# Kernel tuning notes

Hardware: AMD Instinct MI355X
Metric: run time of the kernel (lower is better)

## Reference

```python
import jax, jax.numpy as jnp
import numpy as np

# dims: batch B, n_token T, token_codim D, spatial HxW; channels C = T*D
B, T, D, H, W = 8, 64, 4, 128, 128
C = T * D  # 256
HM1, HM2 = 16, 16  # half of n_modes = (32, 32), per-block kept Fourier modes
EPS = 1e-5  # torch InstanceNorm2d default eps


def setup_inputs() -> dict:
    key = jax.random.key(0)
    ks = jax.random.split(key, 11)
    f = jnp.float32
    sk = 1.0 / (D * D)   # spectral weight init scale (K/Q/V blocks)
    se = 1.0 / (C * C)   # spectral weight init scale (end block)
    return {
        "x": jax.random.normal(ks[0], (B, C, H, W), f),
        "kqv_w1r": jax.random.normal(ks[1], (3, D, D, HM1, HM2), f) * sk,
        "kqv_w1i": jax.random.normal(ks[2], (3, D, D, HM1, HM2), f) * sk,
        "kqv_w2r": jax.random.normal(ks[3], (3, D, D, HM1, HM2), f) * sk,
        "kqv_w2i": jax.random.normal(ks[4], (3, D, D, HM1, HM2), f) * sk,
        "kqv_skip": jax.random.normal(ks[5], (3, D, D), f) * (1.0 / D),
        "end_w1r": jax.random.normal(ks[6], (C, C, HM1, HM2), f) * se,
        "end_w1i": jax.random.normal(ks[7], (C, C, HM1, HM2), f) * se,
        "end_w2r": jax.random.normal(ks[8], (C, C, HM1, HM2), f) * se,
        "end_w2i": jax.random.normal(ks[9], (C, C, HM1, HM2), f) * se,
        "end_skip": jax.random.normal(ks[10], (C, C), f) * (1.0 / C),
    }


def _spectral_conv(x, w1, w2):
    # x: [N, Cin, H, W]; w1/w2: complex [Cin, Cout, HM1, HM2]
    xf = jnp.fft.rfft2(x, norm="forward")  # [N, Cin, H, W//2+1]
    top = jnp.einsum("bixy,ioxy->boxy", xf[:, :, :HM1, :HM2], w1)
    bot = jnp.einsum("bixy,ioxy->boxy", xf[:, :, -HM1:, :HM2], w2)
    out_ft = jnp.zeros((x.shape[0], w1.shape[1], x.shape[2], x.shape[3] // 2 + 1), jnp.complex64)
    out_ft = out_ft.at[:, :, :HM1, :HM2].set(top).at[:, :, -HM1:, :HM2].set(bot)
    return jnp.fft.irfft2(out_ft, s=(x.shape[2], x.shape[3]), norm="forward")


def _fno_block(x, w1, w2, skip):
    # single FNO layer: spectral conv + pointwise linear ('linear' fno_skip), no activation (n_layers=1)
    return _spectral_conv(x, w1, w2) + jnp.einsum("oi,bihw->bohw", skip, x)


def reference(x, kqv_w1r, kqv_w1i, kqv_w2r, kqv_w2i, kqv_skip,
              end_w1r, end_w1i, end_w2r, end_w2i, end_skip):
    # b (t d) h w -> (b t) d h w
    xr = x.reshape(B * T, D, H, W)
    w1 = (kqv_w1r + 1j * kqv_w1i).astype(jnp.complex64)
    w2 = (kqv_w2r + 1j * kqv_w2i).astype(jnp.complex64)
    # stacked K, Q, V FNO blocks over leading axis of size 3
    kqv = jax.vmap(lambda a, b, s: _fno_block(xr, a, b, s))(w1, w2, kqv_skip)  # [3, B*T, D, H, W]
    k, q, v = (t.reshape(B, T, D * H * W) for t in kqv)
    # scaled dot-product attention over tokens (n_head = 1)
    attn = jax.nn.softmax(jnp.einsum("btd,bsd->bts", q, k) / (D * H * W), axis=-1)
    out = jnp.einsum("bts,bsd->btd", attn, v).reshape(B, C, H, W)
    # InstanceNorm2d(affine=False) + exact gelu
    mu = out.mean((-2, -1), keepdims=True)
    var = out.var((-2, -1), keepdims=True)  # biased variance, as in torch eval-mode instance norm
    out = (out - mu) * jax.lax.rsqrt(var + EPS)
    out = jax.nn.gelu(out, approximate=False)
    e1 = (end_w1r + 1j * end_w1i).astype(jnp.complex64)
    e2 = (end_w2r + 1j * end_w2i).astype(jnp.complex64)
    return _fno_block(out, e1, e2, end_skip)
```

## Files before the change

### kernel.cpp

```cpp
#include <hip/hip_runtime.h>
#include <hip/hip_bf16.h>


#define PI2 6.28318530717958647692f

__device__ __forceinline__ float b2f(unsigned short u){ return __uint_as_float(((unsigned)u)<<16); }
__device__ __forceinline__ float lo2f(unsigned u){ return __uint_as_float(u<<16); }
__device__ __forceinline__ float hi2f(unsigned u){ return __uint_as_float(u & 0xffff0000u); }
__device__ __forceinline__ unsigned short f2b(float f){
  unsigned x = __float_as_uint(f);
  x += 0x7fffu + ((x>>16)&1u);
  return (unsigned short)(x>>16);
}
__device__ __forceinline__ unsigned pack2(float a, float b){
  return (unsigned)f2b(a) | ((unsigned)f2b(b)<<16);
}

template<bool F32>
__global__ __launch_bounds__(256)
void k_fwd_dft(const void* __restrict__ srcv,
               float* __restrict__ outr, float* __restrict__ outi)
{
  __shared__ unsigned short xs[16384];
  __shared__ float Xwr[2048], Xwi[2048];
  __shared__ float twc[128], tws[128];
  const int tid = threadIdx.x;
  const long plane = blockIdx.x;
  if (F32){
    const float4* p4 = (const float4*)((const float*)srcv + plane*16384);
    uint2* x2 = (uint2*)xs;
    for (int i=tid;i<4096;i+=256){
      float4 v = p4[i];
      x2[i] = make_uint2(pack2(v.x,v.y), pack2(v.z,v.w));
    }
  } else {
    const uint4* p4 = (const uint4*)((const unsigned short*)srcv + plane*16384);
    uint4* x4 = (uint4*)xs;
    for (int i=tid;i<2048;i+=256) x4[i] = p4[i];
  }
  if (tid < 128){
    float s,c; sincosf((float)tid*(PI2/128.0f), &s, &c);
    twc[tid]=c; tws[tid]=s;
  }
  __syncthreads();
  const unsigned* xu = (const unsigned*)xs;
  for (int o=tid; o<2048; o+=256){
    int h = o >> 4, kx = o & 15;
    const unsigned* row = xu + h*64;
    float ar=0.f, ai=0.f;
    int m0 = 0, m1 = kx;
    const int step = (2*kx) & 127;
    for (int w2=0; w2<64; ++w2){
      unsigned u = row[w2];
      float a0 = lo2f(u), a1 = hi2f(u);
      ar = fmaf(a0, twc[m0], ar); ai = fmaf(-a0, tws[m0], ai);
      ar = fmaf(a1, twc[m1], ar); ai = fmaf(-a1, tws[m1], ai);
      m0 = (m0 + step) & 127; m1 = (m1 + step) & 127;
    }
    Xwr[o]=ar; Xwi[o]=ai;
  }
  __syncthreads();
  for (int o=tid; o<512; o+=256){
    int kyi = o >> 4, kx = o & 15;
    int ky = (kyi < 16) ? kyi : (kyi + 96);
    float ar=0.f, ai=0.f;
    int m = 0;
    const int step = ky & 127;
    for (int h=0; h<128; ++h){
      float A = Xwr[h*16+kx], B = Xwi[h*16+kx];
      float c = twc[m], s = tws[m];
      ar = fmaf(A, c, fmaf( B, s, ar));
      ai = fmaf(B, c, fmaf(-A, s, ai));
      m = (m + step) & 127;
    }
    outr[plane*512+o] = ar * (1.f/16384.f);
    outi[plane*512+o] = ai * (1.f/16384.f);
  }
}

__global__ __launch_bounds__(256)
void k_kqv_synth(const float* __restrict__ xfr, const float* __restrict__ xfi,
                 const float* __restrict__ w1r, const float* __restrict__ w1i,
                 const float* __restrict__ w2r, const float* __restrict__ w2i,
                 const float* __restrict__ skw,
                 const float* __restrict__ x,
                 unsigned short* __restrict__ qkv, int blk_off)
{
  __shared__ float xr_s[2048], xi_s[2048];
  __shared__ float ofr[512], ofi[512];
  __shared__ float Zr[2048], Zi[2048];
  __shared__ float twc[128], tws[128];
  const int tid = threadIdx.x;
  const int slot = blockIdx.x >> 9;
  const int blk  = blk_off + slot;
  const int bt   = blockIdx.x & 511;
  for (int j=tid; j<2048; j+=256){
    xr_s[j] = xfr[(long)bt*2048 + j];
    xi_s[j] = xfi[(long)bt*2048 + j];
  }
  if (tid < 128){
    float s,c; sincosf((float)tid*(PI2/128.0f), &s, &c);
    twc[tid]=c; tws[tid]=s;
  }
  __syncthreads();
  for (int o=0; o<4; ++o){
    for (int m=tid; m<512; m+=256){
      const int top = (m < 256);
      const float* wr = top ? w1r : w2r;
      const float* wi = top ? w1i : w2i;
      const int off = top ? m : (m-256);
      float ar=0.f, ai=0.f;
      #pragma unroll
      for (int i=0;i<4;++i){
        int widx = ((blk*4+i)*4+o)*256 + off;
        float wre = wr[widx], wim = wi[widx];
        float xr = xr_s[i*512+m], xi = xi_s[i*512+m];
        ar += xr*wre - xi*wim;
        ai += xr*wim + xi*wre;
      }
      ofr[m]=ar; ofi[m]=ai;
    }
    __syncthreads();
    for (int z=tid; z<2048; z+=256){
      int h = z >> 4, kx = z & 15;
      float ar=0.f, ai=0.f;
      int m = 0;
      const int step = h;
      #pragma unroll
      for (int kyi=0; kyi<16; ++kyi){
        float A=ofr[kyi*16+kx], B=ofi[kyi*16+kx];
        float c=twc[m], s=tws[m];
        ar = fmaf(A,c,fmaf(-B,s,ar));
        ai = fmaf(A,s,fmaf( B,c,ai));
        m = (m+step)&127;
      }
      m = (112*h)&127;
      #pragma unroll
      for (int kyi=16; kyi<32; ++kyi){
        float A=ofr[kyi*16+kx], B=ofi[kyi*16+kx];
        float c=twc[m], s=tws[m];
        ar = fmaf(A,c,fmaf(-B,s,ar));
        ai = fmaf(A,s,fmaf( B,c,ai));
        m = (m+step)&127;
      }
      float sc = (kx==0) ? 1.f : 2.f;
      Zr[z]=ar*sc; Zi[z]=ai*sc;
    }
    __syncthreads();
    float sk0=skw[(blk*4+o)*4+0];
    float sk1=skw[(blk*4+o)*4+1];
    float sk2=skw[(blk*4+o)*4+2];
    float sk3=skw[(blk*4+o)*4+3];
    const float* xb = x + (long)bt*65536;
    unsigned short* ob = qkv + ((long)(slot*512+bt)*4 + o)*16384;
    for (int pix=tid; pix<16384; pix+=256){
      int h = pix >> 7, w = pix & 127;
      const float* Zrh = Zr + h*16;
      const float* Zih = Zi + h*16;
      float acc = Zrh[0];
      float cw = twc[w], sw = tws[w];
      float cr = cw, si = sw;
      #pragma unroll
      for (int kx=1; kx<16; ++kx){
        acc = fmaf(Zrh[kx], cr, fmaf(-Zih[kx], si, acc));
        float cr2 = cr*cw - si*sw;
        si = fmaf(cr, sw, si*cw);
        cr = cr2;
      }
      acc = fmaf(sk0, xb[pix        ], acc);
      acc = fmaf(sk1, xb[16384 + pix], acc);
      acc = fmaf(sk2, xb[32768 + pix], acc);
      acc = fmaf(sk3, xb[49152 + pix], acc);
      ob[pix] = f2b(acc);
    }
    __syncthreads();
  }
}

__global__ __launch_bounds__(256)
void k_attn_qk(const unsigned short* __restrict__ qkv, float* __restrict__ Sp)
{
  __shared__ unsigned qs[8192], ks[8192];
  const int tid = threadIdx.x;
  const int b = blockIdx.x >> 8, ch = blockIdx.x & 255;
  {
    const unsigned* qg = (const unsigned*)qkv + (long)(512 + b*64)*32768 + ch*128;
    const unsigned* kg = (const unsigned*)qkv + (long)(b*64)*32768 + ch*128;
    for (int i=tid; i<8192; i+=256){
      int t = i >> 7, j = i & 127;
      int sw = j*64 + ((t + j) & 63);
      qs[sw] = qg[(long)t*32768 + j];
      ks[sw] = kg[(long)t*32768 + j];
    }
  }
  __syncthreads();
  const int t0 = (tid >> 4) << 2, s0 = (tid & 15) << 2;
  float acc[16];
  #pragma unroll
  for (int i=0;i<16;++i) acc[i]=0.f;
  for (int j=0; j<128; ++j){
    const unsigned* qrow = qs + j*64;
    const unsigned* krow = ks + j*64;
    float ql[4], qh[4], kl[4], kh[4];
    #pragma unroll
    for (int r=0;r<4;++r){ unsigned u=qrow[(t0+r+j)&63]; ql[r]=lo2f(u); qh[r]=hi2f(u); }
    #pragma unroll
    for (int c=0;c<4;++c){ unsigned u=krow[(s0+c+j)&63]; kl[c]=lo2f(u); kh[c]=hi2f(u); }
    #pragma unroll
    for (int r=0;r<4;++r)
      #pragma unroll
      for (int c=0;c<4;++c)
        acc[r*4+c] = fmaf(ql[r], kl[c], fmaf(qh[r], kh[c], acc[r*4+c]));
  }
  float* out = Sp + (long)(b*256+ch)*4096;
  #pragma unroll
  for (int r=0;r<4;++r)
    #pragma unroll
    for (int c=0;c<4;++c)
      out[(t0+r)*64 + s0+c] = acc[r*4+c];
}

__global__ __launch_bounds__(64)
void k_softmax(const float* __restrict__ Sp, float* __restrict__ attn)
{
  const int s = threadIdx.x;
  const int b = blockIdx.x >> 6, t = blockIdx.x & 63;
  const float* base = Sp + (long)b*1048576 + t*64 + s;
  float acc = 0.f;
  for (int ch=0; ch<256; ++ch) acc += base[(long)ch*4096];
  acc *= (1.f/65536.f);
  float mx = acc;
  #pragma unroll
  for (int off=32; off; off>>=1) mx = fmaxf(mx, __shfl_xor(mx, off));
  float e = __expf(acc - mx);
  float sm = e;
  #pragma unroll
  for (int off=32; off; off>>=1) sm += __shfl_xor(sm, off);
  attn[(long)blockIdx.x*64 + s] = e / sm;
}

__global__ __launch_bounds__(256)
void k_attn_v(const unsigned short* __restrict__ qkv, const float* __restrict__ attn,
              unsigned short* __restrict__ outg)
{
  __shared__ float At[4096];
  const int tid = threadIdx.x;
  const int pt = blockIdx.x & 15, d = (blockIdx.x>>4)&3, b = blockIdx.x>>6;
  for (int i=tid; i<4096; i+=256){
    int s = i >> 6, t = i & 63;
    At[i] = attn[(long)b*4096 + t*64 + s];
  }
  __syncthreads();
  const unsigned short* vb0 = qkv + ((long)(b*64)*4 + d)*16384;
  unsigned short* ob0 = outg + ((long)b*256 + d)*16384;
  for (int pass=0; pass<4; ++pass){
    int p = pt*1024 + pass*256 + tid;
    float acc[64];
    #pragma unroll
    for (int t=0;t<64;++t) acc[t]=0.f;
    for (int s=0; s<64; ++s){
      float vv = b2f(vb0[(long)s*65536 + p]);
      const float4* ar = (const float4*)(At + s*64);
      #pragma unroll
      for (int t4=0; t4<16; ++t4){
        float4 a = ar[t4];
        acc[t4*4+0] = fmaf(a.x, vv, acc[t4*4+0]);
        acc[t4*4+1] = fmaf(a.y, vv, acc[t4*4+1]);
        acc[t4*4+2] = fmaf(a.z, vv, acc[t4*4+2]);
        acc[t4*4+3] = fmaf(a.w, vv, acc[t4*4+3]);
      }
    }
    #pragma unroll
    for (int t=0;t<64;++t) ob0[(long)t*65536 + p] = f2b(acc[t]);
  }
}

__global__ __launch_bounds__(256)
void k_stats(const unsigned short* __restrict__ outg, float* __restrict__ stats)
{
  const int tid = threadIdx.x;
  const long plane = blockIdx.x;
  const unsigned* p = (const unsigned*)(outg + plane*16384);
  float s=0.f, q=0.f;
  for (int i=tid; i<8192; i+=256){
    unsigned u = p[i];
    float a = lo2f(u), b = hi2f(u);
    s += a + b; q = fmaf(a,a,fmaf(b,b,q));
  }
  __shared__ float red[8];
  #pragma unroll
  for (int off=32; off; off>>=1){ s += __shfl_xor(s, off); q += __shfl_xor(q, off); }
  if ((tid & 63) == 0){ red[tid>>6] = s; red[4 + (tid>>6)] = q; }
  __syncthreads();
  if (tid == 0){
    float S = red[0]+red[1]+red[2]+red[3];
    float Q = red[4]+red[5]+red[6]+red[7];
    float mu = S * (1.f/16384.f);
    float var = Q * (1.f/16384.f) - mu*mu;
    stats[plane*2]   = mu;
    stats[plane*2+1] = rsqrtf(var + 1e-5f);
  }
}

__global__ __launch_bounds__(256)
void k_norm_gelu(unsigned short* __restrict__ outg, const float* __restrict__ stats)
{
  unsigned* p = (unsigned*)outg;
  int gi = blockIdx.x*256 + threadIdx.x;
  #pragma unroll
  for (int it=0; it<8; ++it){
    int idx = gi + it*2097152;
    int plane = idx >> 13;
    float mu = stats[plane*2], rs = stats[plane*2+1];
    unsigned u = p[idx];
    float a = (lo2f(u)-mu)*rs, b = (hi2f(u)-mu)*rs;
    a = 0.5f*a*(1.f + erff(a*0.70710678118654752f));
    b = 0.5f*b*(1.f + erff(b*0.70710678118654752f));
    p[idx] = pack2(a, b);
  }
}

__global__ __launch_bounds__(256)
void k_end_mix(const float* __restrict__ gfr, const float* __restrict__ gfi,
               const float* __restrict__ w1r, const float* __restrict__ w1i,
               const float* __restrict__ w2r, const float* __restrict__ w2i,
               float* __restrict__ efr, float* __restrict__ efi)
{
  __shared__ float2 gbuf[2048];
  const int tid = threadIdx.x;
  const int kyi = blockIdx.x >> 4, ot = blockIdx.x & 15;
  const int ol = tid >> 4, kx = tid & 15;
  const int o = ot*16 + ol;
  const float* wr = (kyi < 16) ? w1r : w2r;
  const float* wi = (kyi < 16) ? w1i : w2i;
  const int moff = (kyi & 15)*16 + kx;
  const int mode = kyi*16 + kx;
  float accr[8], acci[8];
  #pragma unroll
  for (int bb=0; bb<8; ++bb){ accr[bb]=0.f; acci[bb]=0.f; }
  for (int ic=0; ic<16; ++ic){
    __syncthreads();
    for (int e=tid; e<2048; e+=256){
      int ii = e >> 7, r = e & 127, bb = r >> 4, k2 = r & 15;
      long gidx = ((long)(bb*256 + ic*16 + ii))*512 + kyi*16 + k2;
      gbuf[e] = make_float2(gfr[gidx], gfi[gidx]);
    }
    __syncthreads();
    #pragma unroll 4
    for (int ii=0; ii<16; ++ii){
      int i = ic*16 + ii;
      long widx = ((long)i*256 + o)*256 + moff;
      float wre = wr[widx], wim = wi[widx];
      #pragma unroll
      for (int bb=0; bb<8; ++bb){
        float2 g = gbuf[ii*128 + bb*16 + kx];
        accr[bb] = fmaf(g.x, wre, fmaf(-g.y, wim, accr[bb]));
        acci[bb] = fmaf(g.x, wim, fmaf( g.y, wre, acci[bb]));
      }
    }
  }
  #pragma unroll
  for (int bb=0; bb<8; ++bb){
    long eidx = ((long)(bb*256 + o))*512 + mode;
    efr[eidx] = accr[bb];
    efi[eidx] = acci[bb];
  }
}

__global__ __launch_bounds__(256)
void k_end_skip_add(const unsigned short* __restrict__ g, const float* __restrict__ skw,
                    float* __restrict__ outp)
{
  __shared__ unsigned short sk[16384];
  const int tid = threadIdx.x;
  const int pt = blockIdx.x & 31, ot = (blockIdx.x>>5)&3, b = blockIdx.x>>7;
  for (int e=tid; e<16384; e+=256){
    int ol = e >> 8, i = e & 255;
    int grp = ol >> 4, w = ol & 15;
    sk[i*64 + (((grp + i)&3)<<4) + w] = f2b(skw[(long)(ot*64+ol)*256 + i]);
  }
  __syncthreads();
  const int to = tid >> 6, tp = tid & 63;
  float acc[16][8];
  #pragma unroll
  for (int j=0;j<16;++j)
    #pragma unroll
    for (int px=0;px<8;++px) acc[j][px]=0.f;
  const uint4* g4 = (const uint4*)g + (long)b*524288 + pt*64 + tp;
  const uint4* skv4 = (const uint4*)sk;
  for (int i=0; i<256; ++i){
    uint4 gv = g4[(long)i*2048];
    float gx[8];
    gx[0]=lo2f(gv.x); gx[1]=hi2f(gv.x); gx[2]=lo2f(gv.y); gx[3]=hi2f(gv.y);
    gx[4]=lo2f(gv.z); gx[5]=hi2f(gv.z); gx[6]=lo2f(gv.w); gx[7]=hi2f(gv.w);
    const uint4* skp = skv4 + i*8 + (((to + i)&3)<<1);
    uint4 s0 = skp[0], s1 = skp[1];
    float sv[16];
    sv[0]=lo2f(s0.x); sv[1]=hi2f(s0.x); sv[2]=lo2f(s0.y); sv[3]=hi2f(s0.y);
    sv[4]=lo2f(s0.z); sv[5]=hi2f(s0.z); sv[6]=lo2f(s0.w); sv[7]=hi2f(s0.w);
    sv[8]=lo2f(s1.x); sv[9]=hi2f(s1.x); sv[10]=lo2f(s1.y); sv[11]=hi2f(s1.y);
    sv[12]=lo2f(s1.z); sv[13]=hi2f(s1.z); sv[14]=lo2f(s1.w); sv[15]=hi2f(s1.w);
    #pragma unroll
    for (int j=0;j<16;++j)
      #pragma unroll
      for (int px=0;px<8;++px)
        acc[j][px] = fmaf(sv[j], gx[px], acc[j][px]);
  }
  #pragma unroll
  for (int j=0;j<16;++j){
    int o = ot*64 + to*16 + j;
    long base = ((long)(b*256 + o))*16384 + pt*512 + tp*8;
    float4* ov = (float4*)(outp + base);
    ov[0] = make_float4(acc[j][0], acc[j][1], acc[j][2], acc[j][3]);
    ov[1] = make_float4(acc[j][4], acc[j][5], acc[j][6], acc[j][7]);
  }
}

__global__ __launch_bounds__(256)
void k_end_idft(const float* __restrict__ efr, const float* __restrict__ efi,
                float* __restrict__ outp)
{
  __shared__ float ofr[512], ofi[512];
  __shared__ float Zr[2048], Zi[2048];
  __shared__ float twc[128], tws[128];
  const int tid = threadIdx.x;
  const long plane = blockIdx.x;
  for (int m=tid; m<512; m+=256){ ofr[m]=efr[plane*512+m]; ofi[m]=efi[plane*512+m]; }
  if (tid < 128){
    float s,c; sincosf((float)tid*(PI2/128.0f), &s, &c);
    twc[tid]=c; tws[tid]=s;
  }
  __syncthreads();
  for (int z=tid; z<2048; z+=256){
    int h = z >> 4, kx = z & 15;
    float ar=0.f, ai=0.f;
    int m = 0;
    const int step = h;
    #pragma unroll
    for (int kyi=0; kyi<16; ++kyi){
      float A=ofr[kyi*16+kx], B=ofi[kyi*16+kx];
      float c=twc[m], s=tws[m];
      ar = fmaf(A,c,fmaf(-B,s,ar));
      ai = fmaf(A,s,fmaf( B,c,ai));
      m = (m+step)&127;
    }
    m = (112*h)&127;
    #pragma unroll
    for (int kyi=16; kyi<32; ++kyi){
      float A=ofr[kyi*16+kx], B=ofi[kyi*16+kx];
      float c=twc[m], s=tws[m];
      ar = fmaf(A,c,fmaf(-B,s,ar));
      ai = fmaf(A,s,fmaf( B,c,ai));
      m = (m+step)&127;
    }
    float sc = (kx==0) ? 1.f : 2.f;
    Zr[z]=ar*sc; Zi[z]=ai*sc;
  }
  __syncthreads();
  for (int pix=tid; pix<16384; pix+=256){
    int h = pix >> 7, w = pix & 127;
    const float* Zrh = Zr + h*16;
    const float* Zih = Zi + h*16;
    float acc = Zrh[0];
    float cw = twc[w], sw = tws[w];
    float cr = cw, si = sw;
    #pragma unroll
    for (int kx=1; kx<16; ++kx){
      acc = fmaf(Zrh[kx], cr, fmaf(-Zih[kx], si, acc));
      float cr2 = cr*cw - si*sw;
      si = fmaf(cr, sw, si*cw);
      cr = cr2;
    }
    outp[plane*16384 + pix] += acc;
  }
}

extern "C" void kernel_launch(void* const* d_in, const int* in_sizes, int n_in,
                              void* d_out, int out_size, void* d_ws, size_t ws_size,
                              hipStream_t stream) {
  const float* x     = (const float*)d_in[0];
  const float* kw1r  = (const float*)d_in[1];
  const float* kw1i  = (const float*)d_in[2];
  const float* kw2r  = (const float*)d_in[3];
  const float* kw2i  = (const float*)d_in[4];
  const float* kskip = (const float*)d_in[5];
  const float* ew1r  = (const float*)d_in[6];
  const float* ew1i  = (const float*)d_in[7];
  const float* ew2r  = (const float*)d_in[8];
  const float* ew2i  = (const float*)d_in[9];
  const float* eskip = (const float*)d_in[10];
  float* outp = (float*)d_out;

  unsigned short* qkv = (unsigned short*)d_out;

  char* ws = (char*)d_ws;
  float* XFr   = (float*)ws;
  float* XFi   = XFr + 1048576;
  float* Sp    = XFi + 1048576;
  float* EFr   = Sp;
  float* EFi   = Sp + 1048576;
  float* attn  = Sp + 8388608;
  float* stats = attn + 32768;
  unsigned short* outg = (unsigned short*)(stats + 4096);

  k_fwd_dft<true>  <<<2048, 256, 0, stream>>>(x, XFr, XFi);
  k_kqv_synth      <<<1024, 256, 0, stream>>>(XFr, XFi, kw1r, kw1i, kw2r, kw2i, kskip, x, qkv, 0);
  k_attn_qk        <<<2048, 256, 0, stream>>>(qkv, Sp);
  k_softmax        <<< 512,  64, 0, stream>>>(Sp, attn);
  k_kqv_synth      <<< 512, 256, 0, stream>>>(XFr, XFi, kw1r, kw1i, kw2r, kw2i, kskip, x, qkv, 2);
  k_attn_v         <<< 512, 256, 0, stream>>>(qkv, attn, outg);
  k_stats          <<<2048, 256, 0, stream>>>(outg, stats);
  k_norm_gelu      <<<8192, 256, 0, stream>>>(outg, stats);
  k_fwd_dft<false> <<<2048, 256, 0, stream>>>(outg, XFr, XFi);
  k_end_mix        <<< 512, 256, 0, stream>>>(XFr, XFi, ew1r, ew1i, ew2r, ew2i, EFr, EFi);
  k_end_skip_add   <<<1024, 256, 0, stream>>>(outg, eskip, outp);
  k_end_idft       <<<2048, 256, 0, stream>>>(EFr, EFi, outp);
}
```

Measured before the change: 2.067 ms.

## Replace scalar end-skip channel mix with bf16 MFMA GEMM kernel

The 256x256 end-block pointwise skip, previously done with scalar FMAs per block, becomes a bf16 MFMA GEMM. It uses double-buffered LDS tiles, with the weight tile loaded through global_load_lds and the activation columns gathered into LDS. A small kernel pre-converts the skip weights to bf16 in workspace so the weight tile is not reconverted in every block. The aim is to move the largest dense matmul onto matrix cores. The cost is strided 16-bit activation gathers and non-vectorized output stores.

```diff
diff --git a/kernel.cpp b/kernel.cpp
--- a/kernel.cpp
+++ b/kernel.cpp
@@ -3,6 +3,9 @@
 
 
 #define PI2 6.28318530717958647692f
+
+typedef float f32x4 __attribute__((ext_vector_type(4)));
+typedef __bf16 bf16x8 __attribute__((ext_vector_type(8)));
 
 __device__ __forceinline__ float b2f(unsigned short u){ return __uint_as_float(((unsigned)u)<<16); }
 __device__ __forceinline__ float lo2f(unsigned u){ return __uint_as_float(u<<16); }
@@ -14,6 +17,10 @@
 }
 __device__ __forceinline__ unsigned pack2(float a, float b){
   return (unsigned)f2b(a) | ((unsigned)f2b(b)<<16);
+}
+__device__ __forceinline__ void glds16(const void* g, void* l){
+  __builtin_amdgcn_global_load_lds((__attribute__((address_space(1))) void*)g,
+                                   (__attribute__((address_space(3))) void*)l, 16, 0, 0);
 }
 
 template<bool F32>
@@ -240,6 +247,15 @@
 }
 
 __global__ __launch_bounds__(256)
+void k_conv_skip(const float* __restrict__ w, unsigned short* __restrict__ o)
+{
+  int i = (blockIdx.x*256 + threadIdx.x)*4;
+  float4 v = *(const float4*)(w + i);
+  uint2 r = make_uint2(pack2(v.x,v.y), pack2(v.z,v.w));
+  *(uint2*)(o + i) = r;
+}
+
+__global__ __launch_bounds__(256)
 void k_attn_v(const unsigned short* __restrict__ qkv, const float* __restrict__ attn,
               unsigned short* __restrict__ outg)
 {
@@ -368,51 +384,89 @@
 }
 
 __global__ __launch_bounds__(256)
-void k_end_skip_add(const unsigned short* __restrict__ g, const float* __restrict__ skw,
-                    float* __restrict__ outp)
-{
-  __shared__ unsigned short sk[16384];
-  const int tid = threadIdx.x;
-  const int pt = blockIdx.x & 31, ot = (blockIdx.x>>5)&3, b = blockIdx.x>>7;
-  for (int e=tid; e<16384; e+=256){
-    int ol = e >> 8, i = e & 255;
-    int grp = ol >> 4, w = ol & 15;
-    sk[i*64 + (((grp + i)&3)<<4) + w] = f2b(skw[(long)(ot*64+ol)*256 + i]);
-  }
-  __syncthreads();
-  const int to = tid >> 6, tp = tid & 63;
-  float acc[16][8];
-  #pragma unroll
-  for (int j=0;j<16;++j)
-    #pragma unroll
-    for (int px=0;px<8;++px) acc[j][px]=0.f;
-  const uint4* g4 = (const uint4*)g + (long)b*524288 + pt*64 + tp;
-  const uint4* skv4 = (const uint4*)sk;
-  for (int i=0; i<256; ++i){
-    uint4 gv = g4[(long)i*2048];
-    float gx[8];
-    gx[0]=lo2f(gv.x); gx[1]=hi2f(gv.x); gx[2]=lo2f(gv.y); gx[3]=hi2f(gv.y);
-    gx[4]=lo2f(gv.z); gx[5]=hi2f(gv.z); gx[6]=lo2f(gv.w); gx[7]=hi2f(gv.w);
-    const uint4* skp = skv4 + i*8 + (((to + i)&3)<<1);
-    uint4 s0 = skp[0], s1 = skp[1];
-    float sv[16];
-    sv[0]=lo2f(s0.x); sv[1]=hi2f(s0.x); sv[2]=lo2f(s0.y); sv[3]=hi2f(s0.y);
-    sv[4]=lo2f(s0.z); sv[5]=hi2f(s0.z); sv[6]=lo2f(s0.w); sv[7]=hi2f(s0.w);
-    sv[8]=lo2f(s1.x); sv[9]=hi2f(s1.x); sv[10]=lo2f(s1.y); sv[11]=hi2f(s1.y);
-    sv[12]=lo2f(s1.z); sv[13]=hi2f(s1.z); sv[14]=lo2f(s1.w); sv[15]=hi2f(s1.w);
-    #pragma unroll
-    for (int j=0;j<16;++j)
-      #pragma unroll
-      for (int px=0;px<8;++px)
-        acc[j][px] = fmaf(sv[j], gx[px], acc[j][px]);
-  }
-  #pragma unroll
-  for (int j=0;j<16;++j){
-    int o = ot*64 + to*16 + j;
-    long base = ((long)(b*256 + o))*16384 + pt*512 + tp*8;
-    float4* ov = (float4*)(outp + base);
-    ov[0] = make_float4(acc[j][0], acc[j][1], acc[j][2], acc[j][3]);
-    ov[1] = make_float4(acc[j][4], acc[j][5], acc[j][6], acc[j][7]);
+void k_end_skip_mfma(const unsigned short* __restrict__ g,
+                     const unsigned short* __restrict__ skb,
+                     float* __restrict__ outp)
+{
+  __shared__ unsigned short As[2][8192];
+  __shared__ unsigned short Bs[2][2048];
+  const int tid  = threadIdx.x;
+  const int lane = tid & 63, wv = tid >> 6;
+  const int l15  = lane & 15, rg = lane >> 4;
+  const int b = blockIdx.x >> 8, pt = blockIdx.x & 255;
+
+  const int bks = tid & 3;
+  const unsigned short* gcol = g + (long)b*4194304 + pt*64 + (tid >> 2);
+
+  const int arow = lane >> 2;
+  const int acol = (lane & 3)*8;
+
+  f32x4 acc[4][4];
+  #pragma unroll
+  for (int mi=0; mi<4; ++mi)
+    #pragma unroll
+    for (int ni=0; ni<4; ++ni) acc[mi][ni] = (f32x4){0.f,0.f,0.f,0.f};
+
+  unsigned br[8];
+  #pragma unroll
+  for (int j=0;j<8;++j) br[j] = gcol[(long)(bks*8 + j)*16384];
+  #pragma unroll
+  for (int q=0;q<4;++q){
+    int row0 = (wv*4+q)*16;
+    glds16(skb + (long)(row0 + arow)*256 + acol, &As[0][row0*32]);
+  }
+  {
+    uint4 v;
+    v.x = br[0]|(br[1]<<16); v.y = br[2]|(br[3]<<16);
+    v.z = br[4]|(br[5]<<16); v.w = br[6]|(br[7]<<16);
+    *(uint4*)&Bs[0][(tid>>2)*32 + bks*8] = v;
+  }
+  __syncthreads();
+
+  #pragma unroll
+  for (int t=0; t<8; ++t){
+    const int cur = t & 1;
+    if (t < 7){
+      #pragma unroll
+      for (int j=0;j<8;++j) br[j] = gcol[(long)((t+1)*32 + bks*8 + j)*16384];
+      #pragma unroll
+      for (int q=0;q<4;++q){
+        int row0 = (wv*4+q)*16;
+        glds16(skb + (long)(row0 + arow)*256 + (t+1)*32 + acol, &As[cur^1][row0*32]);
+      }
+    }
+    bf16x8 af[4], bfr[4];
+    #pragma unroll
+    for (int mi=0;mi<4;++mi)
+      af[mi] = *(const bf16x8*)&As[cur][(wv*64 + mi*16 + l15)*32 + rg*8];
+    #pragma unroll
+    for (int ni=0;ni<4;++ni)
+      bfr[ni] = *(const bf16x8*)&Bs[cur][(ni*16 + l15)*32 + rg*8];
+    #pragma unroll
+    for (int mi=0;mi<4;++mi)
+      #pragma unroll
+      for (int ni=0;ni<4;++ni)
+        acc[mi][ni] = __builtin_amdgcn_mfma_f32_16x16x32_bf16(af[mi], bfr[ni], acc[mi][ni], 0,0,0);
+    if (t < 7){
+      uint4 v;
+      v.x = br[0]|(br[1]<<16); v.y = br[2]|(br[3]<<16);
+      v.z = br[4]|(br[5]<<16); v.w = br[6]|(br[7]<<16);
+      *(uint4*)&Bs[cur^1][(tid>>2)*32 + bks*8] = v;
+    }
+    __syncthreads();
+  }
+
+  float* ob = outp + (long)b*4194304 + pt*64;
+  #pragma unroll
+  for (int mi=0;mi<4;++mi){
+    #pragma unroll
+    for (int r=0;r<4;++r){
+      int m = wv*64 + mi*16 + rg*4 + r;
+      float* orow = ob + (long)m*16384;
+      #pragma unroll
+      for (int ni=0;ni<4;++ni)
+        orow[ni*16 + l15] = acc[mi][ni][r];
+    }
   }
 }
 
@@ -499,6 +553,7 @@
   float* Sp    = XFi + 1048576;
   float* EFr   = Sp;
   float* EFi   = Sp + 1048576;
+  unsigned short* skb = (unsigned short*)(Sp + 3145728);
   float* attn  = Sp + 8388608;
   float* stats = attn + 32768;
   unsigned short* outg = (unsigned short*)(stats + 4096);
@@ -507,12 +562,13 @@
   k_kqv_synth      <<<1024, 256, 0, stream>>>(XFr, XFi, kw1r, kw1i, kw2r, kw2i, kskip, x, qkv, 0);
   k_attn_qk        <<<2048, 256, 0, stream>>>(qkv, Sp);
   k_softmax        <<< 512,  64, 0, stream>>>(Sp, attn);
+  k_conv_skip      <<<  64, 256, 0, stream>>>(eskip, skb);
   k_kqv_synth      <<< 512, 256, 0, stream>>>(XFr, XFi, kw1r, kw1i, kw2r, kw2i, kskip, x, qkv, 2);
   k_attn_v         <<< 512, 256, 0, stream>>>(qkv, attn, outg);
   k_stats          <<<2048, 256, 0, stream>>>(outg, stats);
   k_norm_gelu      <<<8192, 256, 0, stream>>>(outg, stats);
   k_fwd_dft<false> <<<2048, 256, 0, stream>>>(outg, XFr, XFi);
   k_end_mix        <<< 512, 256, 0, stream>>>(XFr, XFi, ew1r, ew1i, ew2r, ew2i, EFr, EFi);
-  k_end_skip_add   <<<1024, 256, 0, stream>>>(outg, eskip, outp);
+  k_end_skip_mfma  <<<2048, 256, 0, stream>>>(outg, skb, outp);
   k_end_idft       <<<2048, 256, 0, stream>>>(EFr, EFi, outp);
 }
```

Result: faster. 1.776 ms (-14.1%).
